# Performance work log

Measured on AMD Instinct MI355X. Metric: run time of the kernel, lower is better.

Reference implementation:

```python
import jax, jax.numpy as jnp
import numpy as np
from jax import lax

B, H, W, Q, C = 2, 96, 96, 30000, 64
DIMS = [C * 9 + 4, 256, 256, 256, 256, 3]  # imnet MLP


def setup_inputs() -> dict:
    key = jax.random.key(0)
    ks = jax.random.split(key, 20)
    d = {}
    d["inp"] = jax.random.normal(ks[0], (B, 3, H, W), jnp.float32)
    d["coord"] = jax.random.uniform(ks[1], (B, Q, 2), jnp.float32) * 2.0 - 1.0
    d["cell"] = jax.random.uniform(ks[2], (B, Q, 2), jnp.float32) * (2.0 / 256.0)
    d["conv_w"] = jax.random.normal(ks[3], (C, 3, 3, 3), jnp.float32) * 0.1
    d["conv_b"] = jnp.zeros((C,), jnp.float32)
    for i in range(5):
        fan_in = DIMS[i]
        d[f"w{i}"] = jax.random.normal(ks[4 + i], (DIMS[i], DIMS[i + 1]), jnp.float32) / np.sqrt(fan_in)
        d[f"b{i}"] = jnp.zeros((DIMS[i + 1],), jnp.float32)
    return d


def _liif_forward(inp, coord, cell, conv_w, conv_b, ws, bs):
    # encoder: 3x3 conv + tanh (gen_feat)
    feat = lax.conv_general_dilated(inp, conv_w, (1, 1), "SAME",
                                    dimension_numbers=("NCHW", "OIHW", "NCHW"))
    feat = jnp.tanh(feat + conv_b[None, :, None, None])  # [B,C,H,W]
    b, c, h, w = feat.shape

    # feat_unfold: F.unfold(feat, 3, padding=1) -> [B, C*9, H, W]
    pad = jnp.pad(feat, ((0, 0), (0, 0), (1, 1), (1, 1)))
    patches = jnp.stack([pad[:, :, i:i + h, j:j + w] for i in range(3) for j in range(3)], axis=2)
    fu = patches.reshape(b, c * 9, h, w).transpose(0, 2, 3, 1)  # [B,H,W,9C]

    # local ensemble offsets
    offsets = jnp.array([[-1., -1.], [-1., 1.], [1., -1.], [1., 1.]], jnp.float32)
    rad = jnp.array([1.0 / h, 1.0 / w], jnp.float32)  # 2/r/2
    eps = 1e-6
    ec = coord[None] + (offsets * rad)[:, None, None, :] + eps  # [4,B,Q,2]
    ec = jnp.clip(ec, -1 + 1e-10, 1 - 1e-10)

    # grid_sample nearest, align_corners=False: ix = ((x+1)*size - 1)/2, round
    iy = jnp.clip(jnp.round((ec[..., 0] + 1) * h / 2 - 0.5).astype(jnp.int32), 0, h - 1)
    ix = jnp.clip(jnp.round((ec[..., 1] + 1) * w / 2 - 0.5).astype(jnp.int32), 0, w - 1)
    b_idx = jnp.arange(b)[None, :, None]  # [1,B,1]
    q_feat = fu[b_idx, iy, ix]  # [4,B,Q,9C]

    # feat_coord (make_coord): pixel-center coords in [-1,1]
    yc = (-1.0 + (2.0 * jnp.arange(h, dtype=jnp.float32) + 1.0) / h)
    xc = (-1.0 + (2.0 * jnp.arange(w, dtype=jnp.float32) + 1.0) / w)
    fc = jnp.stack(jnp.meshgrid(yc, xc, indexing="ij"), axis=-1)  # [H,W,2]
    q_coord = fc[iy, ix]  # [4,B,Q,2]

    scale = jnp.array([h, w], jnp.float32)
    rel_coord = (coord[None] - q_coord) * scale  # [4,B,Q,2]
    rel_cell = cell * scale  # [B,Q,2]

    x = jnp.concatenate(
        [q_feat, rel_coord, jnp.broadcast_to(rel_cell[None], rel_coord.shape)], axis=-1)  # [4,B,Q,580]

    # imnet MLP
    for wi, bi in zip(ws[:-1], bs[:-1]):
        x = jax.nn.relu(x @ wi + bi)
    x = x @ ws[-1] + bs[-1]  # [4,B,Q,3]

    areas = jnp.abs(jnp.prod(rel_coord, axis=-1, keepdims=True)) + 1e-9
    areas = areas / jnp.sum(areas, axis=0, keepdims=True)
    areas = areas[::-1]  # swap diagonal ensemble weights

    out = jnp.sum(x * areas, axis=0)  # [B,Q,3]
    return jnp.tanh(out) * 1.01  # fat_tanh(eps=0.01)


def reference(inp, coord, cell, conv_w, conv_b, w0, b0, w1, b1, w2, b2, w3, b3, w4, b4):
    return _liif_forward(inp, coord, cell, conv_w, conv_b,
                         [w0, w1, w2, w3, w4], [b0, b1, b2, b3, b4])
```

## Files before the change

kernel.cpp:

```cpp
#include <hip/hip_runtime.h>


typedef _Float16 half8   __attribute__((ext_vector_type(8)));
typedef _Float16 half4v  __attribute__((ext_vector_type(4)));
typedef _Float16 half2v  __attribute__((ext_vector_type(2)));
typedef float    float4v __attribute__((ext_vector_type(4)));
typedef float    floatx16 __attribute__((ext_vector_type(16)));

__device__ __forceinline__ _Float16 to_h(float v) {
  return (_Float16)fminf(fmaxf(v, -60000.0f), 60000.0f);
}

#define NQ 30000
#define QT 469
#define QTP 472

__global__ void prep_kernel(const float* __restrict__ w0,
                            const float* __restrict__ w1,
                            const float* __restrict__ w2,
                            const float* __restrict__ w3,
                            const float* __restrict__ w4,
                            _Float16* __restrict__ p0, _Float16* __restrict__ p1,
                            _Float16* __restrict__ p2, _Float16* __restrict__ p3,
                            _Float16* __restrict__ p4) {
  int idx = blockIdx.x * 256 + threadIdx.x;
  if (idx < 18944) {
    int kb = idx >> 8, n = idx & 255;
    half8 hv;
#pragma unroll
    for (int i = 0; i < 8; ++i) {
      int f = kb * 8 + i;
      float v = 0.0f;
      if (f < 576)      v = w0[((f & 63) * 9 + (f >> 6)) * 256 + n];
      else if (f < 580) v = w0[f * 256 + n];
      hv[i] = (_Float16)v;
    }
    *(half8*)(p0 + idx * 8) = hv;
  } else if (idx < 43520) {
    int j = idx - 18944;
    int l = j >> 13;
    int j2 = j & 8191;
    int kb = j2 >> 8, n = j2 & 255;
    const float* w = (l == 0) ? w1 : (l == 1) ? w2 : w3;
    _Float16* p = (l == 0) ? p1 : (l == 1) ? p2 : p3;
    half8 hv;
#pragma unroll
    for (int i = 0; i < 8; ++i)
      hv[i] = (_Float16)w[(kb * 8 + i) * 256 + n];
    *(half8*)(p + j2 * 8) = hv;
  } else if (idx < 44032) {
    int j = idx - 43520;
    int kb = j >> 4, n = j & 15;
    half8 hv;
#pragma unroll
    for (int i = 0; i < 8; ++i) {
      float v = (n < 3) ? w4[(kb * 8 + i) * 3 + n] : 0.0f;
      hv[i] = (_Float16)v;
    }
    *(half8*)(p4 + j * 8) = hv;
  }
}

__global__ void conv_kernel(const float* __restrict__ inp,
                            const float* __restrict__ cw,
                            const float* __restrict__ cb,
                            _Float16* __restrict__ P) {
  __shared__ __align__(16) float s_w[1728];
  __shared__ __align__(16) float s_b[64];
  for (int i = threadIdx.x; i < 1728; i += 256) s_w[i] = cw[i];
  if (threadIdx.x < 64) s_b[threadIdx.x] = cb[threadIdx.x];
  __syncthreads();
  int tid = blockIdx.x * 256 + threadIdx.x;
  if (tid >= 2 * 98 * 98) return;
  int b = tid / 9604;
  int rem = tid % 9604;
  int yy = rem / 98, xx = rem % 98;
  alignas(16) _Float16 outv[64];
  if (yy == 0 || yy == 97 || xx == 0 || xx == 97) {
#pragma unroll
    for (int c = 0; c < 64; ++c) outv[c] = (_Float16)0.0f;
  } else {
    int y = yy - 1, x = xx - 1;
    float win[27];
#pragma unroll
    for (int ci = 0; ci < 3; ++ci)
#pragma unroll
      for (int ky = 0; ky < 3; ++ky)
#pragma unroll
        for (int kx = 0; kx < 3; ++kx) {
          int yi = y + ky - 1, xi = x + kx - 1;
          float v = 0.0f;
          if (yi >= 0 && yi < 96 && xi >= 0 && xi < 96)
            v = inp[((b * 3 + ci) * 96 + yi) * 96 + xi];
          win[ci * 9 + ky * 3 + kx] = v;
        }
    for (int co = 0; co < 64; ++co) {
      float acc = s_b[co];
#pragma unroll
      for (int k = 0; k < 27; ++k) acc = fmaf(win[k], s_w[co * 27 + k], acc);
      outv[co] = (_Float16)tanhf(acc);
    }
  }
  _Float16* dst = P + tid * 64;
#pragma unroll
  for (int j = 0; j < 8; ++j) ((half8*)dst)[j] = ((const half8*)outv)[j];
}

__global__ __launch_bounds__(256, 1) void gmat_kernel(
    const _Float16* __restrict__ P,
    const _Float16* __restrict__ wp0,
    _Float16* __restrict__ G) {
  __shared__ __align__(16) _Float16 s_p[3][98][68];

  const int t    = threadIdx.x;
  const int lane = t & 63;
  const int wv   = t >> 6;
  const int ln32 = lane & 31;
  const int hi   = lane >> 5;
  const int blk  = blockIdx.x;
  const int bb   = (blk & 4) >> 2;
  const int y    = (blk >> 3) * 4 + (blk & 3);

  const int rowbase = (bb * 98 + y) * 98 * 64;
  for (int j = t; j < 2352; j += 256) {
    int row = j / 784;
    int jr  = j - row * 784;
    int px  = jr >> 3;
    int ci  = jr & 7;
    half8 v = *(const half8*)(P + rowbase + row * 6272 + jr * 8);
    *(half8*)(&s_p[row][px][ci * 8]) = v;
  }
  __syncthreads();

  const _Float16* wb0 = wp0 + (hi * 256 + wv * 64 + ln32) * 8;

  floatx16 acc[2][3];
#pragma unroll
  for (int mt2 = 0; mt2 < 2; ++mt2)
#pragma unroll
    for (int nt = 0; nt < 3; ++nt) acc[mt2][nt] = (floatx16)(0.0f);

  half8 afA[2], afB[2];
  afA[0] = *(const half8*)(wb0);          afA[1] = *(const half8*)(wb0 + 256);
  afB[0] = *(const half8*)(wb0 + 4096);   afB[1] = *(const half8*)(wb0 + 4096 + 256);

#pragma unroll 1
  for (int s = 0; s < 36; s += 2) {
    {
      const int patch = s >> 2;
      const int py = patch / 3, px = patch % 3;
      const int cb = ((s & 3) << 4) + hi * 8;
      half8 bf[3];
#pragma unroll
      for (int nt = 0; nt < 3; ++nt)
        bf[nt] = *(const half8*)(&s_p[py][nt * 32 + ln32 + px][cb]);
#pragma unroll
      for (int mt2 = 0; mt2 < 2; ++mt2)
#pragma unroll
        for (int nt = 0; nt < 3; ++nt)
          acc[mt2][nt] = __builtin_amdgcn_mfma_f32_32x32x16_f16(
              afA[mt2], bf[nt], acc[mt2][nt], 0, 0, 0);
      const int sp = (s + 2 <= 35) ? (s + 2) : 35;
      afA[0] = *(const half8*)(wb0 + sp * 4096);
      afA[1] = *(const half8*)(wb0 + sp * 4096 + 256);
    }
    {
      const int s1 = s + 1;
      const int patch = s1 >> 2;
      const int py = patch / 3, px = patch % 3;
      const int cb = ((s1 & 3) << 4) + hi * 8;
      half8 bf[3];
#pragma unroll
      for (int nt = 0; nt < 3; ++nt)
        bf[nt] = *(const half8*)(&s_p[py][nt * 32 + ln32 + px][cb]);
#pragma unroll
      for (int mt2 = 0; mt2 < 2; ++mt2)
#pragma unroll
        for (int nt = 0; nt < 3; ++nt)
          acc[mt2][nt] = __builtin_amdgcn_mfma_f32_32x32x16_f16(
              afB[mt2], bf[nt], acc[mt2][nt], 0, 0, 0);
      const int sp = (s + 3 <= 35) ? (s + 3) : 35;
      afB[0] = *(const half8*)(wb0 + sp * 4096);
      afB[1] = *(const half8*)(wb0 + sp * 4096 + 256);
    }
  }
  const int gybase = ((bb * 98 + y) * 98) * 256;
#pragma unroll
  for (int mt2 = 0; mt2 < 2; ++mt2)
#pragma unroll
    for (int nt = 0; nt < 3; ++nt) {
      half8 c0, c1;
#pragma unroll
      for (int j = 0; j < 8; ++j) {
        c0[j] = (_Float16)acc[mt2][nt][j];
        c1[j] = (_Float16)acc[mt2][nt][8 + j];
      }
      _Float16* ga = G + gybase + (nt * 32 + ln32) * 256 + (wv * 2 + mt2) * 32 + hi * 16;
      *(half8*)(ga)     = c0;
      *(half8*)(ga + 8) = c1;
    }
}

__device__ __forceinline__ void writeback32(floatx16 (&acc)[2][2],
                                            const float* __restrict__ sb,
                                            _Float16 (*s_h)[264],
                                            int wv, int ln32, int hi) {
#pragma unroll
  for (int mt2 = 0; mt2 < 2; ++mt2) {
    const int mb = wv * 64 + mt2 * 32 + 4 * hi;
#pragma unroll
    for (int g = 0; g < 4; ++g) {
      const int m0 = mb + 8 * g;
      float b0 = sb[m0], b1 = sb[m0 + 1], b2 = sb[m0 + 2], b3 = sb[m0 + 3];
#pragma unroll
      for (int nt2 = 0; nt2 < 2; ++nt2) {
        const int n = nt2 * 32 + ln32;
        float v0 = fmaxf(acc[mt2][nt2][4 * g + 0] + b0, 0.0f);
        float v1 = fmaxf(acc[mt2][nt2][4 * g + 1] + b1, 0.0f);
        float v2 = fmaxf(acc[mt2][nt2][4 * g + 2] + b2, 0.0f);
        float v3 = fmaxf(acc[mt2][nt2][4 * g + 3] + b3, 0.0f);
        half2v lo  = __builtin_bit_cast(half2v, __builtin_amdgcn_cvt_pkrtz(v0, v1));
        half2v hi2 = __builtin_bit_cast(half2v, __builtin_amdgcn_cvt_pkrtz(v2, v3));
        half4v hv;
        hv[0] = lo[0]; hv[1] = lo[1]; hv[2] = hi2[0]; hv[3] = hi2[1];
        *(half4v*)(&s_h[n][m0]) = hv;
      }
    }
  }
}

__device__ __forceinline__ void layer256(const _Float16* __restrict__ wbl,
                                         _Float16 (*s_h)[264],
                                         int ln32, int hi,
                                         floatx16 (&acc)[2][2]) {
#pragma unroll
  for (int mt2 = 0; mt2 < 2; ++mt2)
#pragma unroll
    for (int nt2 = 0; nt2 < 2; ++nt2) acc[mt2][nt2] = (floatx16)(0.0f);
  half8 afA[2], afB[2], bfA[2], bfB[2];
  afA[0] = *(const half8*)(wbl);
  afA[1] = *(const half8*)(wbl + 256);
  afB[0] = *(const half8*)(wbl + 4096);
  afB[1] = *(const half8*)(wbl + 4096 + 256);
#pragma unroll
  for (int nt2 = 0; nt2 < 2; ++nt2) {
    bfA[nt2] = *(const half8*)(&s_h[nt2 * 32 + ln32][hi * 8]);
    bfB[nt2] = *(const half8*)(&s_h[nt2 * 32 + ln32][16 + hi * 8]);
  }
#pragma unroll 1
  for (int s = 0; s < 16; s += 2) {
#pragma unroll
    for (int mt2 = 0; mt2 < 2; ++mt2)
#pragma unroll
      for (int nt2 = 0; nt2 < 2; ++nt2)
        acc[mt2][nt2] = __builtin_amdgcn_mfma_f32_32x32x16_f16(
            afA[mt2], bfA[nt2], acc[mt2][nt2], 0, 0, 0);
    {
      const int sc = (s + 2 < 16) ? (s + 2) : 0;
      const int sw = (s + 2 < 16) ? (s + 2) : 15;
      afA[0] = *(const half8*)(wbl + sw * 4096);
      afA[1] = *(const half8*)(wbl + sw * 4096 + 256);
#pragma unroll
      for (int nt2 = 0; nt2 < 2; ++nt2)
        bfA[nt2] = *(const half8*)(&s_h[nt2 * 32 + ln32][sc * 16 + hi * 8]);
    }
#pragma unroll
    for (int mt2 = 0; mt2 < 2; ++mt2)
#pragma unroll
      for (int nt2 = 0; nt2 < 2; ++nt2)
        acc[mt2][nt2] = __builtin_amdgcn_mfma_f32_32x32x16_f16(
            afB[mt2], bfB[nt2], acc[mt2][nt2], 0, 0, 0);
    {
      const int sc = (s + 3 < 16) ? (s + 3) : 0;
      const int sw = (s + 3 < 16) ? (s + 3) : 15;
      afB[0] = *(const half8*)(wbl + sw * 4096);
      afB[1] = *(const half8*)(wbl + sw * 4096 + 256);
#pragma unroll
      for (int nt2 = 0; nt2 < 2; ++nt2)
        bfB[nt2] = *(const half8*)(&s_h[nt2 * 32 + ln32][sc * 16 + hi * 8]);
    }
  }
}

__global__ __launch_bounds__(256, 3) void liif_main(
    const float* __restrict__ coord, const float* __restrict__ cell,
    const float* __restrict__ bias0, const float* __restrict__ bias1,
    const float* __restrict__ bias2, const float* __restrict__ bias3,
    const float* __restrict__ bias4,
    const _Float16* __restrict__ G,
    const _Float16* __restrict__ wp0, const _Float16* __restrict__ wp1,
    const _Float16* __restrict__ wp2, const _Float16* __restrict__ wp3,
    const _Float16* __restrict__ wp4,
    float* __restrict__ out) {
  __shared__ __align__(16) int      s_pix[4][64];
  __shared__ __align__(16) float    s_area[4][64];
  __shared__ __align__(16) _Float16 s_ext[4][64][8];
  __shared__ __align__(16) float    s_bias[1028];
  __shared__ __align__(16) float    s_out[64][4];
  __shared__ __align__(16) float    s_num[64][4];
  __shared__ __align__(16) _Float16 s_h[64][264];

  const int t   = threadIdx.x;
  const int blk = blockIdx.x;
  const int bb  = (blk & 4) >> 2;
  const int tile = (blk >> 3) * 4 + (blk & 3);
  const int q0  = tile * 64;

  for (int i = t; i < 1027; i += 256) {
    float v;
    if (i < 256)       v = bias0[i];
    else if (i < 512)  v = bias1[i - 256];
    else if (i < 768)  v = bias2[i - 512];
    else if (i < 1024) v = bias3[i - 768];
    else               v = bias4[i - 1024];
    s_bias[i] = v;
  }

  if (t < 64) {
    int q = q0 + t;
    bool valid = q < NQ;
    float c0 = 0.f, c1 = 0.f, e0 = 0.f, e1 = 0.f;
    if (valid) {
      int base = (bb * NQ + q) * 2;
      c0 = coord[base]; c1 = coord[base + 1];
      e0 = cell[base];  e1 = cell[base + 1];
    }
    float rc0 = e0 * 96.0f, rc1 = e1 * 96.0f;
#pragma unroll
    for (int o = 0; o < 4; ++o) {
      float oy = (o < 2) ? -1.0f : 1.0f;
      float ox = (o & 1) ? 1.0f : -1.0f;
      float ec0 = (c0 + oy * (1.0f / 96.0f)) + 1e-6f;
      float ec1 = (c1 + ox * (1.0f / 96.0f)) + 1e-6f;
      ec0 = fminf(fmaxf(ec0, -1.0f), 1.0f);
      ec1 = fminf(fmaxf(ec1, -1.0f), 1.0f);
      int iy = (int)rintf(((ec0 + 1.0f) * 96.0f) * 0.5f - 0.5f);
      int ix = (int)rintf(((ec1 + 1.0f) * 96.0f) * 0.5f - 0.5f);
      iy = min(max(iy, 0), 95); ix = min(max(ix, 0), 95);
      float qc0 = -1.0f + (2.0f * (float)iy + 1.0f) / 96.0f;
      float qc1 = -1.0f + (2.0f * (float)ix + 1.0f) / 96.0f;
      float r0 = (c0 - qc0) * 96.0f;
      float r1 = (c1 - qc1) * 96.0f;
      s_pix[o][t]  = (bb * 98 + iy) * 98 + ix;
      s_area[o][t] = fabsf(r0 * r1) + 1e-9f;
      s_ext[o][t][0] = to_h(r0);  s_ext[o][t][1] = to_h(r1);
      s_ext[o][t][2] = to_h(rc0); s_ext[o][t][3] = to_h(rc1);
      s_ext[o][t][4] = (_Float16)0.0f; s_ext[o][t][5] = (_Float16)0.0f;
      s_ext[o][t][6] = (_Float16)0.0f; s_ext[o][t][7] = (_Float16)0.0f;
    }
    s_num[t][0] = 0.f; s_num[t][1] = 0.f; s_num[t][2] = 0.f; s_num[t][3] = 0.f;
  }
  __syncthreads();

  const int lane = t & 63;
  const int wv   = t >> 6;
  const int ln32 = lane & 31;
  const int hi   = lane >> 5;
  const int ln16 = lane & 15;
  const int lg   = lane >> 4;

  const _Float16* wb0 = wp0 + (hi * 256 + wv * 64 + ln32) * 8;
  const _Float16* wb1 = wp1 + (hi * 256 + wv * 64 + ln32) * 8;
  const _Float16* wb2 = wp2 + (hi * 256 + wv * 64 + ln32) * 8;
  const _Float16* wb3 = wp3 + (hi * 256 + wv * 64 + ln32) * 8;

#pragma unroll 1
  for (int p = 0; p < 4; ++p) {
    int pixr[2]; int eidx[2];
#pragma unroll
    for (int nt2 = 0; nt2 < 2; ++nt2) {
      int q = nt2 * 32 + ln32;
      pixr[nt2] = s_pix[p][q];
      eidx[nt2] = (p * 64 + q) * 8;
    }

    floatx16 acc[2][2];
#pragma unroll
    for (int mt2 = 0; mt2 < 2; ++mt2)
#pragma unroll
      for (int nt2 = 0; nt2 < 2; ++nt2) {
        const _Float16* ga = G + pixr[nt2] * 256 + (wv * 2 + mt2) * 32 + hi * 16;
        half8 g0 = *(const half8*)(ga);
        half8 g1 = *(const half8*)(ga + 8);
        floatx16 a;
#pragma unroll
        for (int j = 0; j < 8; ++j) {
          a[j]     = (float)g0[j];
          a[8 + j] = (float)g1[j];
        }
        acc[mt2][nt2] = a;
      }
    {
      half8 ae[2];
      ae[0] = *(const half8*)(wb0 + 36 * 4096);
      ae[1] = *(const half8*)(wb0 + 36 * 4096 + 256);
      half8 z = {(_Float16)0, (_Float16)0, (_Float16)0, (_Float16)0,
                 (_Float16)0, (_Float16)0, (_Float16)0, (_Float16)0};
      half8 bfe[2];
#pragma unroll
      for (int nt2 = 0; nt2 < 2; ++nt2)
        bfe[nt2] = (hi == 0) ? *(const half8*)(&s_ext[0][0][0] + eidx[nt2]) : z;
#pragma unroll
      for (int mt2 = 0; mt2 < 2; ++mt2)
#pragma unroll
        for (int nt2 = 0; nt2 < 2; ++nt2)
          acc[mt2][nt2] = __builtin_amdgcn_mfma_f32_32x32x16_f16(
              ae[mt2], bfe[nt2], acc[mt2][nt2], 0, 0, 0);
    }
    writeback32(acc, s_bias, s_h, wv, ln32, hi);
    __syncthreads();

    layer256(wb1, s_h, ln32, hi, acc);
    __syncthreads();
    writeback32(acc, s_bias + 256, s_h, wv, ln32, hi);
    __syncthreads();

    layer256(wb2, s_h, ln32, hi, acc);
    __syncthreads();
    writeback32(acc, s_bias + 512, s_h, wv, ln32, hi);
    __syncthreads();

    layer256(wb3, s_h, ln32, hi, acc);
    __syncthreads();
    writeback32(acc, s_bias + 768, s_h, wv, ln32, hi);
    __syncthreads();

    half8 af4 = *(const half8*)(wp4 + (lg * 16 + ln16) * 8);
    float4v a4 = (float4v){0.f, 0.f, 0.f, 0.f};
    const int row4 = wv * 16 + ln16;
#pragma unroll 1
    for (int s = 0; s < 8; ++s) {
      half8 afc = af4;
      if (s < 7)
        af4 = *(const half8*)(wp4 + (((s + 1) * 4 + lg) * 16 + ln16) * 8);
      half8 bf = *(const half8*)(&s_h[row4][s * 32 + lg * 8]);
      a4 = __builtin_amdgcn_mfma_f32_16x16x32_f16(afc, bf, a4, 0, 0, 0);
    }
    if (lg == 0) {
      *(float4v*)(&s_out[row4][0]) = a4;
    }
    __syncthreads();

    if (t < 64) {
      float aw = s_area[3 - p][t];
#pragma unroll
      for (int j = 0; j < 3; ++j)
        s_num[t][j] += s_out[t][j] * aw;
    }
  }

  if (t < 64) {
    int q = q0 + t;
    if (q < NQ) {
      float den = s_area[0][t] + s_area[1][t] + s_area[2][t] + s_area[3][t];
      int ob = (bb * NQ + q) * 3;
#pragma unroll
      for (int j = 0; j < 3; ++j) {
        float v = s_num[t][j] / den + s_bias[1024 + j];
        out[ob + j] = tanhf(v) * 1.01f;
      }
    }
  }
}

extern "C" void kernel_launch(void* const* d_in, const int* in_sizes, int n_in,
                              void* d_out, int out_size, void* d_ws, size_t ws_size,
                              hipStream_t stream) {
  const float* inp   = (const float*)d_in[0];
  const float* coord = (const float*)d_in[1];
  const float* cell  = (const float*)d_in[2];
  const float* cw    = (const float*)d_in[3];
  const float* cb    = (const float*)d_in[4];
  const float* w0    = (const float*)d_in[5];
  const float* b0    = (const float*)d_in[6];
  const float* w1    = (const float*)d_in[7];
  const float* b1    = (const float*)d_in[8];
  const float* w2    = (const float*)d_in[9];
  const float* b2    = (const float*)d_in[10];
  const float* w3    = (const float*)d_in[11];
  const float* b3    = (const float*)d_in[12];
  const float* w4    = (const float*)d_in[13];
  const float* b4    = (const float*)d_in[14];

  char* ws = (char*)d_ws;
  _Float16* P   = (_Float16*)(ws);
  _Float16* wp0 = (_Float16*)(ws + 2458624);
  _Float16* wp1 = (_Float16*)(ws + 2761728);
  _Float16* wp2 = (_Float16*)(ws + 2892800);
  _Float16* wp3 = (_Float16*)(ws + 3023872);
  _Float16* wp4 = (_Float16*)(ws + 3154944);
  _Float16* G   = (_Float16*)(ws + 3163136);
  float* outp = (float*)d_out;

  hipLaunchKernelGGL(prep_kernel, dim3(172), dim3(256), 0, stream,
                     w0, w1, w2, w3, w4, wp0, wp1, wp2, wp3, wp4);
  hipLaunchKernelGGL(conv_kernel, dim3(76), dim3(256), 0, stream, inp, cw, cb, P);
  hipLaunchKernelGGL(gmat_kernel, dim3(192), dim3(256), 0, stream, P, wp0, G);
  hipLaunchKernelGGL(liif_main, dim3(8 * (QTP / 4)), dim3(256), 0, stream,
                     coord, cell, b0, b1, b2, b3, b4,
                     G, wp0, wp1, wp2, wp3, wp4, outp);
}
```

Baseline: 301.6 us.

## Process two ensemble offsets concurrently with 512-thread blocks

Doubles the block to eight waves and splits them into two groups, each running the MLP on a different local-ensemble offset. The offset loop shrinks from four iterations to two, and the shared hidden buffer and output staging double to hold both offsets. The aim is fewer block-wide barriers per query tile and more MFMA work in flight per block. In exchange, LDS use per block roughly doubles and the launch bound of 512 threads with a minimum of 4 blocks may constrain registers and occupancy.

```diff
diff --git a/kernel.cpp b/kernel.cpp
--- a/kernel.cpp
+++ b/kernel.cpp
@@ -204,17 +204,17 @@
 __device__ __forceinline__ void writeback32(floatx16 (&acc)[2][2],
                                             const float* __restrict__ sb,
                                             _Float16 (*s_h)[264],
-                                            int wv, int ln32, int hi) {
+                                            int wv_m, int wv_n, int ln32, int hi) {
 #pragma unroll
   for (int mt2 = 0; mt2 < 2; ++mt2) {
-    const int mb = wv * 64 + mt2 * 32 + 4 * hi;
+    const int mb = wv_m * 64 + mt2 * 32 + 4 * hi;
 #pragma unroll
     for (int g = 0; g < 4; ++g) {
       const int m0 = mb + 8 * g;
       float b0 = sb[m0], b1 = sb[m0 + 1], b2 = sb[m0 + 2], b3 = sb[m0 + 3];
 #pragma unroll
       for (int nt2 = 0; nt2 < 2; ++nt2) {
-        const int n = nt2 * 32 + ln32;
+        const int n = wv_n * 64 + nt2 * 32 + ln32;
         float v0 = fmaxf(acc[mt2][nt2][4 * g + 0] + b0, 0.0f);
         float v1 = fmaxf(acc[mt2][nt2][4 * g + 1] + b1, 0.0f);
         float v2 = fmaxf(acc[mt2][nt2][4 * g + 2] + b2, 0.0f);
@@ -231,7 +231,7 @@
 
 __device__ __forceinline__ void layer256(const _Float16* __restrict__ wbl,
                                          _Float16 (*s_h)[264],
-                                         int ln32, int hi,
+                                         int wv_n, int ln32, int hi,
                                          floatx16 (&acc)[2][2]) {
 #pragma unroll
   for (int mt2 = 0; mt2 < 2; ++mt2)
@@ -244,8 +244,8 @@
   afB[1] = *(const half8*)(wbl + 4096 + 256);
 #pragma unroll
   for (int nt2 = 0; nt2 < 2; ++nt2) {
-    bfA[nt2] = *(const half8*)(&s_h[nt2 * 32 + ln32][hi * 8]);
-    bfB[nt2] = *(const half8*)(&s_h[nt2 * 32 + ln32][16 + hi * 8]);
+    bfA[nt2] = *(const half8*)(&s_h[wv_n * 64 + nt2 * 32 + ln32][hi * 8]);
+    bfB[nt2] = *(const half8*)(&s_h[wv_n * 64 + nt2 * 32 + ln32][16 + hi * 8]);
   }
 #pragma unroll 1
   for (int s = 0; s < 16; s += 2) {
@@ -262,7 +262,7 @@
       afA[1] = *(const half8*)(wbl + sw * 4096 + 256);
 #pragma unroll
       for (int nt2 = 0; nt2 < 2; ++nt2)
-        bfA[nt2] = *(const half8*)(&s_h[nt2 * 32 + ln32][sc * 16 + hi * 8]);
+        bfA[nt2] = *(const half8*)(&s_h[wv_n * 64 + nt2 * 32 + ln32][sc * 16 + hi * 8]);
     }
 #pragma unroll
     for (int mt2 = 0; mt2 < 2; ++mt2)
@@ -277,12 +277,12 @@
       afB[1] = *(const half8*)(wbl + sw * 4096 + 256);
 #pragma unroll
       for (int nt2 = 0; nt2 < 2; ++nt2)
-        bfB[nt2] = *(const half8*)(&s_h[nt2 * 32 + ln32][sc * 16 + hi * 8]);
-    }
-  }
-}
-
-__global__ __launch_bounds__(256, 3) void liif_main(
+        bfB[nt2] = *(const half8*)(&s_h[wv_n * 64 + nt2 * 32 + ln32][sc * 16 + hi * 8]);
+    }
+  }
+}
+
+__global__ __launch_bounds__(512, 4) void liif_main(
     const float* __restrict__ coord, const float* __restrict__ cell,
     const float* __restrict__ bias0, const float* __restrict__ bias1,
     const float* __restrict__ bias2, const float* __restrict__ bias3,
@@ -296,9 +296,9 @@
   __shared__ __align__(16) float    s_area[4][64];
   __shared__ __align__(16) _Float16 s_ext[4][64][8];
   __shared__ __align__(16) float    s_bias[1028];
-  __shared__ __align__(16) float    s_out[64][4];
+  __shared__ __align__(16) float    s_out[128][4];
   __shared__ __align__(16) float    s_num[64][4];
-  __shared__ __align__(16) _Float16 s_h[64][264];
+  __shared__ __align__(16) _Float16 s_h[128][264];
 
   const int t   = threadIdx.x;
   const int blk = blockIdx.x;
@@ -306,7 +306,7 @@
   const int tile = (blk >> 3) * 4 + (blk & 3);
   const int q0  = tile * 64;
 
-  for (int i = t; i < 1027; i += 256) {
+  for (int i = t; i < 1027; i += 512) {
     float v;
     if (i < 256)       v = bias0[i];
     else if (i < 512)  v = bias1[i - 256];
@@ -353,25 +353,28 @@
   __syncthreads();
 
   const int lane = t & 63;
-  const int wv   = t >> 6;
+  const int w8   = t >> 6;
+  const int wv_m = w8 & 3;
+  const int wv_n = w8 >> 2;
   const int ln32 = lane & 31;
   const int hi   = lane >> 5;
   const int ln16 = lane & 15;
   const int lg   = lane >> 4;
 
-  const _Float16* wb0 = wp0 + (hi * 256 + wv * 64 + ln32) * 8;
-  const _Float16* wb1 = wp1 + (hi * 256 + wv * 64 + ln32) * 8;
-  const _Float16* wb2 = wp2 + (hi * 256 + wv * 64 + ln32) * 8;
-  const _Float16* wb3 = wp3 + (hi * 256 + wv * 64 + ln32) * 8;
+  const _Float16* wb0 = wp0 + (hi * 256 + wv_m * 64 + ln32) * 8;
+  const _Float16* wb1 = wp1 + (hi * 256 + wv_m * 64 + ln32) * 8;
+  const _Float16* wb2 = wp2 + (hi * 256 + wv_m * 64 + ln32) * 8;
+  const _Float16* wb3 = wp3 + (hi * 256 + wv_m * 64 + ln32) * 8;
 
 #pragma unroll 1
-  for (int p = 0; p < 4; ++p) {
+  for (int p = 0; p < 2; ++p) {
     int pixr[2]; int eidx[2];
+    const int o = p * 2 + wv_n;
 #pragma unroll
     for (int nt2 = 0; nt2 < 2; ++nt2) {
       int q = nt2 * 32 + ln32;
-      pixr[nt2] = s_pix[p][q];
-      eidx[nt2] = (p * 64 + q) * 8;
+      pixr[nt2] = s_pix[o][q];
+      eidx[nt2] = (o * 64 + q) * 8;
     }
 
     floatx16 acc[2][2];
@@ -379,7 +382,7 @@
     for (int mt2 = 0; mt2 < 2; ++mt2)
 #pragma unroll
       for (int nt2 = 0; nt2 < 2; ++nt2) {
-        const _Float16* ga = G + pixr[nt2] * 256 + (wv * 2 + mt2) * 32 + hi * 16;
+        const _Float16* ga = G + pixr[nt2] * 256 + (wv_m * 2 + mt2) * 32 + hi * 16;
         half8 g0 = *(const half8*)(ga);
         half8 g1 = *(const half8*)(ga + 8);
         floatx16 a;
@@ -407,27 +410,27 @@
           acc[mt2][nt2] = __builtin_amdgcn_mfma_f32_32x32x16_f16(
               ae[mt2], bfe[nt2], acc[mt2][nt2], 0, 0, 0);
     }
-    writeback32(acc, s_bias, s_h, wv, ln32, hi);
-    __syncthreads();
-
-    layer256(wb1, s_h, ln32, hi, acc);
-    __syncthreads();
-    writeback32(acc, s_bias + 256, s_h, wv, ln32, hi);
-    __syncthreads();
-
-    layer256(wb2, s_h, ln32, hi, acc);
-    __syncthreads();
-    writeback32(acc, s_bias + 512, s_h, wv, ln32, hi);
-    __syncthreads();
-
-    layer256(wb3, s_h, ln32, hi, acc);
-    __syncthreads();
-    writeback32(acc, s_bias + 768, s_h, wv, ln32, hi);
+    writeback32(acc, s_bias, s_h, wv_m, wv_n, ln32, hi);
+    __syncthreads();
+
+    layer256(wb1, s_h, wv_n, ln32, hi, acc);
+    __syncthreads();
+    writeback32(acc, s_bias + 256, s_h, wv_m, wv_n, ln32, hi);
+    __syncthreads();
+
+    layer256(wb2, s_h, wv_n, ln32, hi, acc);
+    __syncthreads();
+    writeback32(acc, s_bias + 512, s_h, wv_m, wv_n, ln32, hi);
+    __syncthreads();
+
+    layer256(wb3, s_h, wv_n, ln32, hi, acc);
+    __syncthreads();
+    writeback32(acc, s_bias + 768, s_h, wv_m, wv_n, ln32, hi);
     __syncthreads();
 
     half8 af4 = *(const half8*)(wp4 + (lg * 16 + ln16) * 8);
     float4v a4 = (float4v){0.f, 0.f, 0.f, 0.f};
-    const int row4 = wv * 16 + ln16;
+    const int row4 = w8 * 16 + ln16;
 #pragma unroll 1
     for (int s = 0; s < 8; ++s) {
       half8 afc = af4;
@@ -442,10 +445,11 @@
     __syncthreads();
 
     if (t < 64) {
-      float aw = s_area[3 - p][t];
+      float a_lo = s_area[3 - 2 * p][t];
+      float a_hi = s_area[2 - 2 * p][t];
 #pragma unroll
       for (int j = 0; j < 3; ++j)
-        s_num[t][j] += s_out[t][j] * aw;
+        s_num[t][j] += s_out[t][j] * a_lo + s_out[64 + t][j] * a_hi;
     }
   }
 
@@ -496,7 +500,7 @@
                      w0, w1, w2, w3, w4, wp0, wp1, wp2, wp3, wp4);
   hipLaunchKernelGGL(conv_kernel, dim3(76), dim3(256), 0, stream, inp, cw, cb, P);
   hipLaunchKernelGGL(gmat_kernel, dim3(192), dim3(256), 0, stream, P, wp0, G);
-  hipLaunchKernelGGL(liif_main, dim3(8 * (QTP / 4)), dim3(256), 0, stream,
+  hipLaunchKernelGGL(liif_main, dim3(8 * (QTP / 4)), dim3(512), 0, stream,
                      coord, cell, b0, b1, b2, b3, b4,
                      G, wp0, wp1, wp2, wp3, wp4, outp);
 }
```

Result: faster. 285.4 us (-5.4%).
